# Optimization experiments

Measured on AMD Instinct MI355X. Metric: run time of the kernel, lower is better.

## Reference

```python
import jax, jax.numpy as jnp
import numpy as np

DIM = 32
B, H, W = 4, 256, 256


def conv1x1(x, w, b):
    # x: [B,C,H,W], w: [O,C], b: [O]
    return jnp.einsum('bchw,oc->bohw', x, w) + b[None, :, None, None]


def conv3x3(x, w, b):
    # x: [B,C,H,W], w: [O,C,3,3]
    out = jax.lax.conv_general_dilated(
        x, w, window_strides=(1, 1), padding='SAME',
        dimension_numbers=('NCHW', 'OIHW', 'NCHW'))
    return out + b[None, :, None, None]


def fft2d(x):
    # fft2 over last two dims, then fftshift over ALL dims (torch default)
    f = jnp.fft.fftshift(jnp.fft.fft2(x, norm='ortho'))
    return jnp.concatenate([f.real, f.imag], axis=1)  # [B,2C,H,W]


def ifft2d(x):
    f = jnp.fft.ifftshift(x)  # over ALL dims (torch default)
    re, im = jnp.split(f, 2, axis=1)
    c = jax.lax.complex(re, im)
    return jnp.abs(jnp.fft.ifft2(c, norm='ortho'))  # [B,C,H,W]


def setup_inputs() -> dict:
    key = jax.random.key(0)
    ks = jax.random.split(key, 16)
    C = DIM
    s = 0.02  # small init keeps the global-HW dot products in a sane softmax range
    inp = {
        'x': jax.random.normal(ks[0], (B, C, H, W), jnp.float32),
        'y': jax.random.normal(ks[1], (B, C, H, W), jnp.float32),
        'wq': jax.random.normal(ks[2], (C, C), jnp.float32) * s,
        'bq': jnp.zeros((C,), jnp.float32),
        'wk': jax.random.normal(ks[3], (C, C), jnp.float32) * s,
        'bk': jnp.zeros((C,), jnp.float32),
        'wv': jax.random.normal(ks[4], (C, C), jnp.float32) * s,
        'bv': jnp.zeros((C,), jnp.float32),
        'wd': jax.random.normal(ks[5], (C, C), jnp.float32) * s,
        'bd': jnp.zeros((C,), jnp.float32),
        'wc': jax.random.normal(ks[6], (2 * C, 2 * C, 3, 3), jnp.float32) * s,
        'bc': jnp.zeros((2 * C,), jnp.float32),
        'wi': jax.random.normal(ks[7], (2 * C, 2 * C, 3, 3), jnp.float32) * s,
        'bi': jnp.zeros((2 * C,), jnp.float32),
    }
    return inp


def reference(x, y, wq, bq, wk, bk, wv, bv, wd, bd, wc, bc, wi, bi):
    b, c, h, w = x.shape
    xq = conv1x1(x, wq, bq).reshape(b, c, h * w)            # [B,C,HW]
    dft = conv3x3(fft2d(conv1x1(y, wd, bd)), wc, bc)        # [B,2C,H,W]
    yk, yv = jnp.split(dft, 2, axis=1)
    yk = conv1x1(yk, wk, bk).reshape(b, c, h * w)
    yv = conv1x1(yv, wv, bv).reshape(b, c, h * w)
    att = jnp.einsum('bcn,bdn->bcd', xq, yk)                # [B,C,C]
    att = jax.nn.softmax(att, axis=1)                       # softmax over dim=1 (as in torch)
    out = jnp.einsum('bcd,bdn->bcn', att, yv).reshape(b, c, h, w)
    out = out + ifft2d(conv3x3(jax.nn.relu(dft), wi, bi))
    return out
```

## Files before the change

kernel.cpp:

```cpp
#include <hip/hip_runtime.h>
#include <math.h>

#define HW_ (256*256)
#define CH 32
#define CH2 64
#define BATCH 4

typedef short bf16x8 __attribute__((ext_vector_type(8)));
typedef float f32x4 __attribute__((ext_vector_type(4)));

__device__ __forceinline__ unsigned short f2bf(float f) {
    union { float f; unsigned u; } v; v.f = f;
    unsigned r = v.u + 0x7fffu + ((v.u >> 16) & 1u);
    return (unsigned short)(r >> 16);
}
__device__ __forceinline__ float bf2f(unsigned h) {
    union { unsigned u; float f; } v; v.u = h << 16;
    return v.f;
}

__device__ __forceinline__ int ctof_slot(int s) {
    return s < 16 ? s + 16 : s < 32 ? s + 32 : s < 48 ? s - 32 : s - 16;
}

__device__ __forceinline__ float2 cmul(float2 a, float2 b) {
    return make_float2(a.x*b.x - a.y*b.y, a.x*b.y + a.y*b.x);
}

__device__ __forceinline__ uint4 relu_bf16x8(uint4 v) {
    unsigned* pv = (unsigned*)&v;
    #pragma unroll
    for (int q = 0; q < 4; ++q) {
        unsigned a = pv[q];
        unsigned lo = a & 0xffffu, hi = a >> 16;
        if (lo & 0x8000u) lo = 0;
        if (hi & 0x8000u) hi = 0;
        pv[q] = lo | (hi << 16);
    }
    return v;
}

__device__ __forceinline__ void build_tw4(float2* tw, float sign) {
    int tid = threadIdx.x;
    float ang = sign * 6.2831853071795864769f * (float)tid / 256.0f;
    float s, c; sincosf(ang, &s, &c);
    tw[tid] = make_float2(c, s);
}

template<int SGN>
__device__ __forceinline__ void fft16_reg(float2* x, const float2* tw) {
    float2 u[16];
    #pragma unroll
    for (int m0 = 0; m0 < 4; ++m0) {
        float2 x0 = x[m0], x1 = x[m0+4], x2 = x[m0+8], x3 = x[m0+12];
        float2 t0 = make_float2(x0.x+x2.x, x0.y+x2.y);
        float2 t1 = make_float2(x0.x-x2.x, x0.y-x2.y);
        float2 t2 = make_float2(x1.x+x3.x, x1.y+x3.y);
        float2 t3 = make_float2(x1.x-x3.x, x1.y-x3.y);
        float2 r  = make_float2(-SGN*t3.y, SGN*t3.x);
        u[m0*4+0] = make_float2(t0.x+t2.x, t0.y+t2.y);
        u[m0*4+1] = make_float2(t1.x+r.x,  t1.y+r.y);
        u[m0*4+2] = make_float2(t0.x-t2.x, t0.y-t2.y);
        u[m0*4+3] = make_float2(t1.x-r.x,  t1.y-r.y);
    }
    #pragma unroll
    for (int m0 = 1; m0 < 4; ++m0)
        #pragma unroll
        for (int a = 1; a < 4; ++a)
            u[m0*4+a] = cmul(u[m0*4+a], tw[(16*m0*a) & 255]);
    #pragma unroll
    for (int a = 0; a < 4; ++a) {
        float2 x0 = u[a], x1 = u[4+a], x2 = u[8+a], x3 = u[12+a];
        float2 t0 = make_float2(x0.x+x2.x, x0.y+x2.y);
        float2 t1 = make_float2(x0.x-x2.x, x0.y-x2.y);
        float2 t2 = make_float2(x1.x+x3.x, x1.y+x3.y);
        float2 t3 = make_float2(x1.x-x3.x, x1.y-x3.y);
        float2 r  = make_float2(-SGN*t3.y, SGN*t3.x);
        x[a]    = make_float2(t0.x+t2.x, t0.y+t2.y);
        x[a+4]  = make_float2(t1.x+r.x,  t1.y+r.y);
        x[a+8]  = make_float2(t0.x-t2.x, t0.y-t2.y);
        x[a+12] = make_float2(t1.x-r.x,  t1.y-r.y);
    }
}

template<int SGN>
__device__ __forceinline__ void fft_core16(float2* A, const float2* tw) {
    const int tid = threadIdx.x;
    const int l = tid >> 4;
    const int d = tid & 15;
    const int base = l*257;
    float2 x[16];
    #pragma unroll
    for (int n1 = 0; n1 < 16; ++n1) x[n1] = A[base + n1*16 + d];
    fft16_reg<SGN>(x, tw);
    #pragma unroll
    for (int k0 = 1; k0 < 16; ++k0) x[k0] = cmul(x[k0], tw[d*k0]);
    #pragma unroll
    for (int k0 = 0; k0 < 16; ++k0) A[base + k0*16 + ((d + k0) & 15)] = x[k0];
    __syncthreads();
    #pragma unroll
    for (int n0 = 0; n0 < 16; ++n0) x[n0] = A[base + d*16 + ((n0 + d) & 15)];
    fft16_reg<SGN>(x, tw);
    #pragma unroll
    for (int k1 = 0; k1 < 16; ++k1) A[base + d + k1*16] = x[k1];
    __syncthreads();
}

__global__ __launch_bounds__(256) void k_fft_fwd1(const unsigned short* __restrict__ yd, ushort2* __restrict__ CAt) {
    __shared__ float2 A[16*257];
    __shared__ float2 tw[256];
    build_tw4(tw, -1.0f);
    int blk = blockIdx.x;
    int bc = blk >> 4, h0 = (blk & 15) << 4;
    const float sc = 1.0f/16.0f;
    const unsigned short* src = yd + (size_t)bc*HW_ + (size_t)h0*256;
    for (int idx = threadIdx.x; idx < 16*64; idx += 256) {
        int l = idx >> 6, w4 = (idx & 63) << 2;
        uint2 v = *(const uint2*)(src + l*256 + w4);
        A[l*257 + w4+0] = make_float2(bf2f(v.x & 0xffffu)*sc, 0.0f);
        A[l*257 + w4+1] = make_float2(bf2f(v.x >> 16)*sc, 0.0f);
        A[l*257 + w4+2] = make_float2(bf2f(v.y & 0xffffu)*sc, 0.0f);
        A[l*257 + w4+3] = make_float2(bf2f(v.y >> 16)*sc, 0.0f);
    }
    __syncthreads();
    fft_core16<-1>(A, tw);
    int t = threadIdx.x;
    unsigned short pk[32];
    #pragma unroll
    for (int l = 0; l < 16; ++l) {
        float2 v = A[l*257 + t];
        pk[2*l]   = f2bf(v.x);
        pk[2*l+1] = f2bf(v.y);
    }
    uint4* d4 = (uint4*)(CAt + (size_t)bc*HW_ + (size_t)t*256 + h0);
    const uint4* s4 = (const uint4*)pk;
    d4[0] = s4[0]; d4[1] = s4[1]; d4[2] = s4[2]; d4[3] = s4[3];
}

__global__ __launch_bounds__(256) void k_fft_fwd2(const ushort2* __restrict__ CAt, unsigned short* __restrict__ FSH) {
    __shared__ float2 A[16*257];
    __shared__ float2 tw[256];
    build_tw4(tw, -1.0f);
    int blk = blockIdx.x;
    int b = blk >> 9, chalf = (blk >> 8) & 1, w = blk & 255;
    const float sc = 1.0f/16.0f;
    const ushort2* src = CAt + (((size_t)(b*32 + chalf*16))*256 + w)*256;
    for (int idx = threadIdx.x; idx < 16*256; idx += 256) {
        int l = idx >> 8, h = idx & 255;
        ushort2 v = src[(size_t)l*HW_ + h];
        A[l*257 + h] = make_float2(bf2f(v.x)*sc, bf2f(v.y)*sc);
    }
    __syncthreads();
    fft_core16<-1>(A, tw);
    int t = threadIdx.x;
    int bt = (b + 2) & 3;
    int ht = (t + 128) & 255;
    int wt = (w + 128) & 255;
    unsigned short pk[32];
    #pragma unroll
    for (int l = 0; l < 16; ++l) {
        float2 v = A[l*257 + t];
        pk[l]      = f2bf(v.x);
        pk[16 + l] = f2bf(v.y);
    }
    unsigned short* dst = FSH + ((((size_t)bt*256 + ht)*256 + wt)*64 + chalf*32);
    uint4* d4 = (uint4*)dst;
    const uint4* s4 = (const uint4*)pk;
    d4[0] = s4[0]; d4[1] = s4[1]; d4[2] = s4[2]; d4[3] = s4[3];
}

__global__ __launch_bounds__(256) void k_wpack2(const float* __restrict__ wc, const float* __restrict__ wi,
                                                unsigned short* __restrict__ d1, unsigned short* __restrict__ d2) {
    int i = blockIdx.x*256 + threadIdx.x;
    int half = i >= 36864;
    int j = i - half*36864;
    int tap = j >> 12, rem = j & 4095, oc = rem >> 6, s = rem & 63;
    if (half) {
        d2[j] = f2bf(wi[((size_t)(oc*64 + s))*9 + tap]);
    } else {
        int ic = ctof_slot(s);
        d1[j] = f2bf(wc[((size_t)(oc*64 + ic))*9 + tap]);
    }
}

template<int MODE>
__global__ __launch_bounds__(256) void k_conv3(const unsigned short* __restrict__ in_cl,
                                               const unsigned short* __restrict__ wpk,
                                               const float* __restrict__ bias,
                                               unsigned short* __restrict__ outp) {
    __shared__ __align__(16) char Xs[2112*16];
    __shared__ __align__(16) char Ws[1536*16];
    int tid = threadIdx.x;
    int blk = blockIdx.x;
    int wseg = blk & 3, hg = (blk >> 2) & 63, b = blk >> 8;
    int h0 = hg*4, w0 = wseg*64;

    const uint4* wsrc = (const uint4*)wpk;

    for (int gl = tid; gl < 2112; gl += 256) {
        int slot = gl / 528;
        int rem  = gl - slot*528;
        int col  = rem >> 3, hseg = rem & 7;
        int hh = h0 - 1 + slot;
        int wcol = w0 - 1 + col;
        uint4 v = make_uint4(0,0,0,0);
        if (hh >= 0 && hh < 256 && wcol >= 0 && wcol < 256) {
            v = *(const uint4*)(in_cl + (((size_t)(b*256 + hh)*256 + wcol)*64) + hseg*8);
            if (MODE == 1) v = relu_bf16x8(v);
        }
        *(uint4*)(Xs + ((gl << 4) ^ ((col & 7) << 4))) = v;
    }
    #pragma unroll
    for (int q = 0; q < 6; ++q) {
        int gw = tid + q*256;
        int oc = (gw >> 3) & 63;
        *(uint4*)(Ws + ((gw << 4) ^ ((oc & 7) << 4))) = wsrc[gw];
    }
    __syncthreads();

    int lane = tid & 63;
    int wv = tid >> 6;
    int l16 = lane & 15, lq = lane >> 4;

    f32x4 acc[4][4];
    #pragma unroll
    for (int i = 0; i < 4; ++i)
        #pragma unroll
        for (int j = 0; j < 4; ++j) acc[i][j] = (f32x4)0.0f;

    for (int dy = 0; dy < 3; ++dy) {
        uint4 xr0 = make_uint4(0,0,0,0), xr1 = make_uint4(0,0,0,0), xr2 = make_uint4(0,0,0,0);
        uint4 wr[6];
        if (dy < 2) {
            int hh = h0 + dy + 2;
            bool hv = hh < 256;
            {
                int gl = tid;
                int col = gl >> 3, hseg = gl & 7;
                int wcol = w0 - 1 + col;
                if (hv && wcol >= 0 && wcol < 256)
                    xr0 = *(const uint4*)(in_cl + (((size_t)(b*256 + hh)*256 + wcol)*64) + hseg*8);
            }
            {
                int gl = tid + 256;
                int col = gl >> 3, hseg = gl & 7;
                int wcol = w0 - 1 + col;
                if (hv && wcol >= 0 && wcol < 256)
                    xr1 = *(const uint4*)(in_cl + (((size_t)(b*256 + hh)*256 + wcol)*64) + hseg*8);
            }
            if (tid < 16) {
                int gl = tid + 512;
                int col = gl >> 3, hseg = gl & 7;
                int wcol = w0 - 1 + col;
                if (hv && wcol < 256)
                    xr2 = *(const uint4*)(in_cl + (((size_t)(b*256 + hh)*256 + wcol)*64) + hseg*8);
            }
            #pragma unroll
            for (int q = 0; q < 6; ++q)
                wr[q] = wsrc[(dy+1)*1536 + tid + q*256];
        }

        int slot = (wv + dy) & 3;
        #pragma unroll
        for (int dx = 0; dx < 3; ++dx) {
            #pragma unroll
            for (int kk = 0; kk < 2; ++kk) {
                int hseg = kk*4 + lq;
                bf16x8 xf[4], wf[4];
                #pragma unroll
                for (int j = 0; j < 4; ++j) {
                    int col = j*16 + l16 + dx;
                    int g = slot*528 + col*8 + hseg;
                    xf[j] = *(const bf16x8*)(Xs + ((g << 4) ^ ((col & 7) << 4)));
                }
                #pragma unroll
                for (int i = 0; i < 4; ++i) {
                    int oc = i*16 + l16;
                    int lw = dx*512 + oc*8 + hseg;
                    wf[i] = *(const bf16x8*)(Ws + ((lw << 4) ^ ((oc & 7) << 4)));
                    #pragma unroll
                    for (int j = 0; j < 4; ++j) {
                        if (MODE == 0)
                            acc[i][j] = __builtin_amdgcn_mfma_f32_16x16x32_bf16(wf[i], xf[j], acc[i][j], 0, 0, 0);
                        else
                            acc[i][j] = __builtin_amdgcn_mfma_f32_16x16x32_bf16(xf[j], wf[i], acc[i][j], 0, 0, 0);
                    }
                }
            }
        }

        if (dy < 2) {
            __syncthreads();
            int slotn = (dy + 3) & 3;
            {
                int gl = tid;
                int col = gl >> 3;
                uint4 v = (MODE == 1) ? relu_bf16x8(xr0) : xr0;
                int g = slotn*528 + gl;
                *(uint4*)(Xs + ((g << 4) ^ ((col & 7) << 4))) = v;
            }
            {
                int gl = tid + 256;
                int col = gl >> 3;
                uint4 v = (MODE == 1) ? relu_bf16x8(xr1) : xr1;
                int g = slotn*528 + gl;
                *(uint4*)(Xs + ((g << 4) ^ ((col & 7) << 4))) = v;
            }
            if (tid < 16) {
                int gl = tid + 512;
                int col = gl >> 3;
                uint4 v = (MODE == 1) ? relu_bf16x8(xr2) : xr2;
                int g = slotn*528 + gl;
                *(uint4*)(Xs + ((g << 4) ^ ((col & 7) << 4))) = v;
            }
            #pragma unroll
            for (int q = 0; q < 6; ++q) {
                int gw = tid + q*256;
                int oc = (gw >> 3) & 63;
                *(uint4*)(Ws + ((gw << 4) ^ ((oc & 7) << 4))) = wr[q];
            }
            __syncthreads();
        }
    }

    int h = h0 + wv;
    if (MODE == 0) {
        #pragma unroll
        for (int j = 0; j < 4; ++j) {
            int px = w0 + j*16 + l16;
            unsigned short* orow = outp + (((size_t)b*256 + h)*256 + px)*64;
            #pragma unroll
            for (int i = 0; i < 4; ++i) {
                int oc0 = i*16 + lq*4;
                float4 bv = *(const float4*)(bias + oc0);
                unsigned short c0 = f2bf(acc[i][j][0] + bv.x);
                unsigned short c1 = f2bf(acc[i][j][1] + bv.y);
                unsigned short c2 = f2bf(acc[i][j][2] + bv.z);
                unsigned short c3 = f2bf(acc[i][j][3] + bv.w);
                uint2 u;
                u.x = (unsigned)c0 | ((unsigned)c1 << 16);
                u.y = (unsigned)c2 | ((unsigned)c3 << 16);
                *(uint2*)(orow + oc0) = u;
            }
        }
    } else {
        #pragma unroll
        for (int i = 0; i < 4; ++i) {
            int oc = i*16 + l16;
            float bv = bias[oc];
            unsigned short* oplane = outp + ((size_t)b*64 + oc)*HW_ + (size_t)h*256;
            #pragma unroll
            for (int j = 0; j < 4; ++j) {
                int px0 = w0 + j*16 + lq*4;
                unsigned short c0 = f2bf(acc[i][j][0] + bv);
                unsigned short c1 = f2bf(acc[i][j][1] + bv);
                unsigned short c2 = f2bf(acc[i][j][2] + bv);
                unsigned short c3 = f2bf(acc[i][j][3] + bv);
                uint2 u;
                u.x = (unsigned)c0 | ((unsigned)c1 << 16);
                u.y = (unsigned)c2 | ((unsigned)c3 << 16);
                *(uint2*)(oplane + px0) = u;
            }
        }
    }
}

__global__ __launch_bounds__(256) void k_conv1x1(const float* __restrict__ in, const float* __restrict__ w,
                                                 const float* __restrict__ bias, unsigned short* __restrict__ out) {
    __shared__ float ts[32*257];
    int blk = blockIdx.x; int b = blk >> 8, h = blk & 255;
    int tid = threadIdx.x;
    const float* src = in + (size_t)b*CH*HW_ + (size_t)h*256;
    for (int idx = tid; idx < 32*256; idx += 256) {
        int c = idx >> 8, ww = idx & 255;
        ts[c*257 + ww] = src[(size_t)c*HW_ + ww];
    }
    __syncthreads();
    float acc[32];
    #pragma unroll
    for (int o = 0; o < 32; ++o) acc[o] = bias[o];
    for (int c = 0; c < 32; ++c) {
        float v = ts[c*257 + tid];
        #pragma unroll
        for (int o = 0; o < 32; ++o) acc[o] += w[o*32 + c] * v;
    }
    unsigned short* dst = out + (size_t)b*CH*HW_ + (size_t)h*256 + tid;
    #pragma unroll
    for (int o = 0; o < 32; ++o) dst[(size_t)o*HW_] = f2bf(acc[o]);
}

__global__ __launch_bounds__(256) void k_gram(const float* __restrict__ x, const unsigned short* __restrict__ dcl,
                                              float* __restrict__ Mpart, float* __restrict__ Sxp, float* __restrict__ Sdp) {
    __shared__ float mred[1024];
    __shared__ float sxred[32];
    __shared__ float sdred[32];
    int blk = blockIdx.x;
    int b = blk >> 7, chunk = blk & 127;
    int tid = threadIdx.x, lane = tid & 63, wv = tid >> 6;
    int l16 = lane & 15, lq = lane >> 4;
    for (int idx = tid; idx < 1024; idx += 256) mred[idx] = 0.0f;
    if (tid < 32) { sxred[tid] = 0.0f; sdred[tid] = 0.0f; }
    __syncthreads();

    const float* xb0 = x + (size_t)b*CH*HW_ + (size_t)l16*HW_;
    const float* xb1 = xb0 + (size_t)16*HW_;
    const unsigned short* db = dcl + (size_t)b*HW_*64;

    f32x4 acc[2][2];
    #pragma unroll
    for (int i = 0; i < 2; ++i)
        #pragma unroll
        for (int j = 0; j < 2; ++j) acc[i][j] = (f32x4)0.0f;
    float sx0 = 0, sx1 = 0, sd0 = 0, sd1 = 0;

    int pxw = chunk*512 + wv*128;
    #pragma unroll
    for (int ks = 0; ks < 4; ++ks) {
        int px = pxw + ks*32 + lq*8;
        float4 xa = *(const float4*)(xb0 + px);
        float4 xc = *(const float4*)(xb0 + px + 4);
        float4 ya = *(const float4*)(xb1 + px);
        float4 yc = *(const float4*)(xb1 + px + 4);
        bf16x8 a0, a1, b0, b1;
        const float* pxa = (const float*)&xa;
        const float* pxc = (const float*)&xc;
        const float* pya = (const float*)&ya;
        const float* pyc = (const float*)&yc;
        #pragma unroll
        for (int j = 0; j < 4; ++j) {
            a0[j]   = (short)f2bf(pxa[j]);  sx0 += pxa[j];
            a0[4+j] = (short)f2bf(pxc[j]);  sx0 += pxc[j];
            a1[j]   = (short)f2bf(pya[j]);  sx1 += pya[j];
            a1[4+j] = (short)f2bf(pyc[j]);  sx1 += pyc[j];
        }
        const unsigned short* dbp = db + (size_t)px*64 + l16;
        #pragma unroll
        for (int j = 0; j < 8; ++j) {
            unsigned short v0 = dbp[j*64];
            unsigned short v1 = dbp[j*64 + 16];
            b0[j] = (short)v0;  sd0 += bf2f(v0);
            b1[j] = (short)v1;  sd1 += bf2f(v1);
        }
        acc[0][0] = __builtin_amdgcn_mfma_f32_16x16x32_bf16(a0, b0, acc[0][0], 0, 0, 0);
        acc[0][1] = __builtin_amdgcn_mfma_f32_16x16x32_bf16(a0, b1, acc[0][1], 0, 0, 0);
        acc[1][0] = __builtin_amdgcn_mfma_f32_16x16x32_bf16(a1, b0, acc[1][0], 0, 0, 0);
        acc[1][1] = __builtin_amdgcn_mfma_f32_16x16x32_bf16(a1, b1, acc[1][1], 0, 0, 0);
    }

    #pragma unroll
    for (int fi = 0; fi < 2; ++fi)
        #pragma unroll
        for (int fj = 0; fj < 2; ++fj)
            #pragma unroll
            for (int r = 0; r < 4; ++r)
                atomicAdd(&mred[(fi*16 + lq*4 + r)*32 + fj*16 + l16], acc[fi][fj][r]);

    sx0 += __shfl_xor(sx0, 16); sx0 += __shfl_xor(sx0, 32);
    sx1 += __shfl_xor(sx1, 16); sx1 += __shfl_xor(sx1, 32);
    sd0 += __shfl_xor(sd0, 16); sd0 += __shfl_xor(sd0, 32);
    sd1 += __shfl_xor(sd1, 16); sd1 += __shfl_xor(sd1, 32);
    if (lane < 16) {
        atomicAdd(&sxred[l16], sx0);
        atomicAdd(&sxred[l16 + 16], sx1);
        atomicAdd(&sdred[l16], sd0);
        atomicAdd(&sdred[l16 + 16], sd1);
    }
    __syncthreads();

    float* mp = Mpart + ((size_t)(b*128 + chunk))*1024;
    for (int idx = tid; idx < 1024; idx += 256) mp[idx] = mred[idx];
    if (tid < 32) {
        Sxp[(b*128 + chunk)*32 + tid] = sxred[tid];
        Sdp[(b*128 + chunk)*32 + tid] = sdred[tid];
    }
}

__global__ __launch_bounds__(256) void k_att(const float* __restrict__ Mpart, const float* __restrict__ Sxp,
                                              const float* __restrict__ Sdp,
                                              const float* __restrict__ wq, const float* __restrict__ bq,
                                              const float* __restrict__ wk, const float* __restrict__ bk,
                                              const float* __restrict__ wv, const float* __restrict__ bv,
                                              float* __restrict__ att2, float* __restrict__ sout) {
    __shared__ float Mls[1024], T1[1024], attls[32*33];
    __shared__ float wqs[1024], wks[1024], wvs[1024];
    __shared__ float q1[32], k1[32], sxs[32], sds[32];
    int tid = threadIdx.x;
    int b = blockIdx.x;
    for (int idx = tid; idx < 1024; idx += 256) { wqs[idx] = wq[idx]; wks[idx] = wk[idx]; wvs[idx] = wv[idx]; }
    #pragma unroll
    for (int q = 0; q < 4; ++q) {
        int o = tid + q*256;
        float s = 0;
        for (int c = 0; c < 128; ++c) s += Mpart[((size_t)(b*128 + c))*1024 + o];
        Mls[o] = s;
    }
    if (tid < 32) { float s = 0; for (int c = 0; c < 128; ++c) s += Sxp[(b*128 + c)*32 + tid]; sxs[tid] = s; }
    else if (tid < 64) { int e = tid - 32; float s = 0; for (int c = 0; c < 128; ++c) s += Sdp[(b*128 + c)*32 + e]; sds[e] = s; }
    __syncthreads();
    if (tid < 32) { float s=0; for (int a=0;a<32;++a) s += wqs[tid*32+a]*sxs[a]; q1[tid]=s; }
    else if (tid < 64) { int d=tid-32; float s=0; for (int e=0;e<32;++e) s += wks[d*32+e]*sds[e]; k1[d]=s; }
    for (int idx = tid; idx < 1024; idx += 256) {
        int c = idx >> 5, e = idx & 31;
        float s = 0;
        for (int a=0;a<32;++a) s += wqs[c*32+a]*Mls[a*32+e];
        T1[idx] = s;
    }
    __syncthreads();
    for (int idx = tid; idx < 1024; idx += 256) {
        int c = idx >> 5, d = idx & 31;
        float s = 0;
        for (int e=0;e<32;++e) s += T1[c*32+e]*wks[d*32+e];
        s += bq[c]*k1[d] + bk[d]*q1[c] + 65536.0f*bq[c]*bk[d];
        attls[c*33+d] = s;
    }
    __syncthreads();
    if (tid < 32) {
        int d = tid;
        float mx = -1e30f;
        for (int c=0;c<32;++c) mx = fmaxf(mx, attls[c*33+d]);
        float sum = 0;
        for (int c=0;c<32;++c) { float e_ = expf(attls[c*33+d]-mx); attls[c*33+d]=e_; sum+=e_; }
        float inv = 1.0f/sum;
        for (int c=0;c<32;++c) attls[c*33+d] *= inv;
    }
    __syncthreads();
    for (int idx = tid; idx < 1024; idx += 256) {
        int c = idx >> 5, e = idx & 31;
        float s = 0;
        for (int d=0; d<32; ++d) s += attls[c*33+d]*wvs[d*32+e];
        att2[b*1024 + idx] = s;
    }
    if (tid < 32) {
        float s=0; for (int d=0;d<32;++d) s += attls[tid*33+d]*bv[d];
        sout[b*32+tid] = s;
    }
}

__global__ __launch_bounds__(256) void k_fft_inv1(const unsigned short* __restrict__ G, ushort2* __restrict__ Z1T) {
    __shared__ float2 A[16*257];
    __shared__ float2 tw[256];
    build_tw4(tw, 1.0f);
    int blk = blockIdx.x;
    int bc = blk >> 4, w0 = (blk & 15) << 4;
    int b = bc >> 5, c = bc & 31;
    int bs = (b + 2) & 3;
    const float sc = 1.0f/16.0f;
    const unsigned short* gre = G + ((size_t)(bs*CH2 + c + 32))*HW_;
    const unsigned short* gim = G + ((size_t)(bs*CH2 + c))*HW_;
    for (int idx = threadIdx.x; idx < 16*256; idx += 256) {
        int h = idx >> 4, l = idx & 15;
        int hs = (h + 128) & 255;
        int ws = (w0 + l + 128) & 255;
        A[l*257 + h] = make_float2(bf2f(gre[(size_t)hs*256 + ws])*sc, bf2f(gim[(size_t)hs*256 + ws])*sc);
    }
    __syncthreads();
    fft_core16<1>(A, tw);
    ushort2* dst = Z1T + (size_t)bc*HW_;
    for (int idx = threadIdx.x; idx < 16*256; idx += 256) {
        int l = idx >> 8, h = idx & 255;
        float2 v = A[l*257 + h];
        dst[(size_t)(w0 + l)*256 + h] = make_ushort2(f2bf(v.x), f2bf(v.y));
    }
}

__global__ __launch_bounds__(256) void k_fft_inv2(const ushort2* __restrict__ Z1T, unsigned short* __restrict__ Mag) {
    __shared__ float2 A[16*257];
    __shared__ float2 tw[256];
    build_tw4(tw, 1.0f);
    int blk = blockIdx.x;
    int bc = blk >> 4, h0 = (blk & 15) << 4;
    const float sc = 1.0f/16.0f;
    const ushort2* src = Z1T + (size_t)bc*HW_ + h0;
    for (int idx = threadIdx.x; idx < 16*256; idx += 256) {
        int w = idx >> 4, l = idx & 15;
        ushort2 v = src[(size_t)w*256 + l];
        A[l*257 + w] = make_float2(bf2f(v.x)*sc, bf2f(v.y)*sc);
    }
    __syncthreads();
    fft_core16<1>(A, tw);
    unsigned short* dst = Mag + (size_t)bc*HW_ + (size_t)h0*256;
    for (int idx = threadIdx.x; idx < 16*256; idx += 256) {
        int l = idx >> 8, w = idx & 255;
        float2 v = A[l*257 + w];
        dst[l*256 + w] = f2bf(sqrtf(v.x*v.x + v.y*v.y));
    }
}

__global__ __launch_bounds__(256) void k_out(const unsigned short* __restrict__ dcl, const float* __restrict__ att2,
                                             const float* __restrict__ sv, const unsigned short* __restrict__ Mag,
                                             float* __restrict__ out) {
    __shared__ __align__(16) float A2ls[1024];
    __shared__ float svls[32];
    int blk = blockIdx.x; int b = blk >> 8, h = blk & 255;
    int tid = threadIdx.x;
    for (int idx = tid; idx < 1024; idx += 256) A2ls[idx] = att2[b*1024 + idx];
    if (tid < 32) svls[tid] = sv[b*32 + tid];
    __syncthreads();
    int px = tid;
    const uint4* dvp = (const uint4*)(dcl + ((((size_t)b*256 + h)*256 + px)*64 + 32));
    uint4 d0 = dvp[0], d1 = dvp[1];
    unsigned u[8] = {d0.x, d0.y, d0.z, d0.w, d1.x, d1.y, d1.z, d1.w};
    float dv[32];
    #pragma unroll
    for (int i = 0; i < 8; ++i) {
        dv[2*i]   = bf2f(u[i] & 0xffffu);
        dv[2*i+1] = bf2f(u[i] >> 16);
    }
    float accv[32];
    #pragma unroll
    for (int c = 0; c < 32; ++c) accv[c] = svls[c];
    #pragma unroll
    for (int q = 0; q < 8; ++q) {
        #pragma unroll
        for (int c = 0; c < 32; ++c) {
            float4 a4 = *(const float4*)&A2ls[c*32 + q*4];
            accv[c] += a4.x*dv[q*4] + a4.y*dv[q*4+1] + a4.z*dv[q*4+2] + a4.w*dv[q*4+3];
        }
    }
    const unsigned short* mb = Mag + (size_t)b*CH*HW_ + (size_t)h*256 + px;
    float* ob = out + (size_t)b*CH*HW_ + (size_t)h*256 + px;
    #pragma unroll
    for (int c = 0; c < 32; ++c) ob[(size_t)c*HW_] = accv[c] + bf2f(mb[(size_t)c*HW_]);
}

extern "C" void kernel_launch(void* const* d_in, const int* in_sizes, int n_in,
                              void* d_out, int out_size, void* d_ws, size_t ws_size,
                              hipStream_t stream) {
    const float* x  = (const float*)d_in[0];
    const float* y  = (const float*)d_in[1];
    const float* wq = (const float*)d_in[2];
    const float* bq = (const float*)d_in[3];
    const float* wk = (const float*)d_in[4];
    const float* bk = (const float*)d_in[5];
    const float* wv = (const float*)d_in[6];
    const float* bv = (const float*)d_in[7];
    const float* wd = (const float*)d_in[8];
    const float* bd = (const float*)d_in[9];
    const float* wc = (const float*)d_in[10];
    const float* bc = (const float*)d_in[11];
    const float* wi = (const float*)d_in[12];
    const float* bi = (const float*)d_in[13];
    float* out = (float*)d_out;

    char* ws = (char*)d_ws;
    size_t o = 0;
    unsigned short* R1   = (unsigned short*)(ws + o); o += (size_t)BATCH*CH*HW_*2;
    ushort2*        CAt  = (ushort2*)(ws + o);        o += (size_t)BATCH*CH*HW_*4;
    unsigned short* FSHc = (unsigned short*)(ws + o); o += (size_t)BATCH*CH2*HW_*2;
    unsigned short* DFTc = (unsigned short*)(ws + o); o += (size_t)BATCH*CH2*HW_*2;
    unsigned short* Gpl  = (unsigned short*)(ws + o); o += (size_t)BATCH*CH2*HW_*2;
    unsigned short* wpk1 = (unsigned short*)(ws + o); o += 9*64*64*2;
    unsigned short* wpk2 = (unsigned short*)(ws + o); o += 9*64*64*2;
    float*          Mpart= (float*)(ws + o);          o += (size_t)512*1024*4;
    float*          Sxp  = (float*)(ws + o);          o += 512*32*4;
    float*          Sdp  = (float*)(ws + o);          o += 512*32*4;
    float*          A2b  = (float*)(ws + o);          o += 4096*4;
    float*          Svb  = (float*)(ws + o);          o += 128*4;
    if (ws_size < o) return;

    ushort2*        Z1T = CAt;
    unsigned short* Mag = R1;

    k_wpack2<<<288, 256, 0, stream>>>(wc, wi, wpk1, wpk2);
    k_conv1x1<<<1024, 256, 0, stream>>>(y, wd, bd, R1);
    k_fft_fwd1<<<2048, 256, 0, stream>>>(R1, CAt);
    k_fft_fwd2<<<2048, 256, 0, stream>>>(CAt, FSHc);
    k_conv3<0><<<1024, 256, 0, stream>>>(FSHc, wpk1, bc, DFTc);
    k_conv3<1><<<1024, 256, 0, stream>>>(DFTc, wpk2, bi, Gpl);
    k_gram<<<512, 256, 0, stream>>>(x, DFTc, Mpart, Sxp, Sdp);
    k_att<<<4, 256, 0, stream>>>(Mpart, Sxp, Sdp, wq, bq, wk, bk, wv, bv, A2b, Svb);
    k_fft_inv1<<<2048, 256, 0, stream>>>(Gpl, Z1T);
    k_fft_inv2<<<2048, 256, 0, stream>>>(Z1T, Mag);
    k_out<<<1024, 256, 0, stream>>>(DFTc, A2b, Svb, Mag, out);
}
```

Measured before the change: 278.3 us.

## Stage conv3 epilogue and gram inputs through LDS, fuse weight pack into conv1x1

The conv3 epilogue now writes its tile into swizzled shared memory, then issues coalesced 16-byte global stores for both the channel-last and planar output layouts. k_gram stages x and DFT tiles in shared memory per 128-pixel step, so the strided 2-byte gathers from the channel-last buffer become vector loads plus an LDS transpose. The weight-pack kernel is merged into the conv1x1 launch as extra blocks, removing one launch. The cost is extra LDS traffic and more barriers in both kernels.

```diff
diff --git a/kernel.cpp b/kernel.cpp
--- a/kernel.cpp
+++ b/kernel.cpp
@@ -169,18 +169,44 @@
     d4[0] = s4[0]; d4[1] = s4[1]; d4[2] = s4[2]; d4[3] = s4[3];
 }
 
-__global__ __launch_bounds__(256) void k_wpack2(const float* __restrict__ wc, const float* __restrict__ wi,
-                                                unsigned short* __restrict__ d1, unsigned short* __restrict__ d2) {
-    int i = blockIdx.x*256 + threadIdx.x;
-    int half = i >= 36864;
-    int j = i - half*36864;
-    int tap = j >> 12, rem = j & 4095, oc = rem >> 6, s = rem & 63;
-    if (half) {
-        d2[j] = f2bf(wi[((size_t)(oc*64 + s))*9 + tap]);
-    } else {
-        int ic = ctof_slot(s);
-        d1[j] = f2bf(wc[((size_t)(oc*64 + ic))*9 + tap]);
-    }
+__global__ __launch_bounds__(256) void k_conv1x1w(const float* __restrict__ in, const float* __restrict__ w,
+                                                  const float* __restrict__ bias, unsigned short* __restrict__ out,
+                                                  const float* __restrict__ wc, const float* __restrict__ wi,
+                                                  unsigned short* __restrict__ d1, unsigned short* __restrict__ d2) {
+    __shared__ float ts[32*257];
+    int blk = blockIdx.x;
+    int tid = threadIdx.x;
+    if (blk >= 1024) {
+        int i = (blk - 1024)*256 + tid;
+        int half = i >= 36864;
+        int j = i - half*36864;
+        int tap = j >> 12, rem = j & 4095, oc = rem >> 6, s = rem & 63;
+        if (half) {
+            d2[j] = f2bf(wi[((size_t)(oc*64 + s))*9 + tap]);
+        } else {
+            int ic = ctof_slot(s);
+            d1[j] = f2bf(wc[((size_t)(oc*64 + ic))*9 + tap]);
+        }
+        return;
+    }
+    int b = blk >> 8, h = blk & 255;
+    const float* src = in + (size_t)b*CH*HW_ + (size_t)h*256;
+    for (int idx = tid; idx < 32*256; idx += 256) {
+        int c = idx >> 8, ww = idx & 255;
+        ts[c*257 + ww] = src[(size_t)c*HW_ + ww];
+    }
+    __syncthreads();
+    float acc[32];
+    #pragma unroll
+    for (int o = 0; o < 32; ++o) acc[o] = bias[o];
+    for (int c = 0; c < 32; ++c) {
+        float v = ts[c*257 + tid];
+        #pragma unroll
+        for (int o = 0; o < 32; ++o) acc[o] += w[o*32 + c] * v;
+    }
+    unsigned short* dst = out + (size_t)b*CH*HW_ + (size_t)h*256 + tid;
+    #pragma unroll
+    for (int o = 0; o < 32; ++o) dst[(size_t)o*HW_] = f2bf(acc[o]);
 }
 
 template<int MODE>
@@ -323,12 +349,13 @@
         }
     }
 
-    int h = h0 + wv;
+    __syncthreads();
+    char* Es = Xs;
     if (MODE == 0) {
         #pragma unroll
         for (int j = 0; j < 4; ++j) {
-            int px = w0 + j*16 + l16;
-            unsigned short* orow = outp + (((size_t)b*256 + h)*256 + px)*64;
+            int px = j*16 + l16;
+            int rowswz = (px & 7) << 4;
             #pragma unroll
             for (int i = 0; i < 4; ++i) {
                 int oc0 = i*16 + lq*4;
@@ -340,18 +367,19 @@
                 uint2 u;
                 u.x = (unsigned)c0 | ((unsigned)c1 << 16);
                 u.y = (unsigned)c2 | ((unsigned)c3 << 16);
-                *(uint2*)(orow + oc0) = u;
+                int byte = wv*8192 + px*128 + oc0*2;
+                *(uint2*)(Es + (byte ^ rowswz)) = u;
             }
         }
     } else {
         #pragma unroll
         for (int i = 0; i < 4; ++i) {
             int oc = i*16 + l16;
+            int rowswz = (oc & 7) << 4;
             float bv = bias[oc];
-            unsigned short* oplane = outp + ((size_t)b*64 + oc)*HW_ + (size_t)h*256;
             #pragma unroll
             for (int j = 0; j < 4; ++j) {
-                int px0 = w0 + j*16 + lq*4;
+                int px0 = j*16 + lq*4;
                 unsigned short c0 = f2bf(acc[i][j][0] + bv);
                 unsigned short c1 = f2bf(acc[i][j][1] + bv);
                 unsigned short c2 = f2bf(acc[i][j][2] + bv);
@@ -359,38 +387,31 @@
                 uint2 u;
                 u.x = (unsigned)c0 | ((unsigned)c1 << 16);
                 u.y = (unsigned)c2 | ((unsigned)c3 << 16);
-                *(uint2*)(oplane + px0) = u;
-            }
-        }
-    }
-}
-
-__global__ __launch_bounds__(256) void k_conv1x1(const float* __restrict__ in, const float* __restrict__ w,
-                                                 const float* __restrict__ bias, unsigned short* __restrict__ out) {
-    __shared__ float ts[32*257];
-    int blk = blockIdx.x; int b = blk >> 8, h = blk & 255;
-    int tid = threadIdx.x;
-    const float* src = in + (size_t)b*CH*HW_ + (size_t)h*256;
-    for (int idx = tid; idx < 32*256; idx += 256) {
-        int c = idx >> 8, ww = idx & 255;
-        ts[c*257 + ww] = src[(size_t)c*HW_ + ww];
-    }
-    __syncthreads();
-    float acc[32];
-    #pragma unroll
-    for (int o = 0; o < 32; ++o) acc[o] = bias[o];
-    for (int c = 0; c < 32; ++c) {
-        float v = ts[c*257 + tid];
-        #pragma unroll
-        for (int o = 0; o < 32; ++o) acc[o] += w[o*32 + c] * v;
-    }
-    unsigned short* dst = out + (size_t)b*CH*HW_ + (size_t)h*256 + tid;
-    #pragma unroll
-    for (int o = 0; o < 32; ++o) dst[(size_t)o*HW_] = f2bf(acc[o]);
+                int byte = wv*8192 + oc*128 + px0*2;
+                *(uint2*)(Es + (byte ^ rowswz)) = u;
+            }
+        }
+    }
+    __syncthreads();
+    #pragma unroll
+    for (int q = 0; q < 8; ++q) {
+        int off = (q*256 + tid)*16;
+        uint4 v = *(const uint4*)(Es + (off ^ (((off >> 7) & 7) << 4)));
+        int wvp = off >> 13;
+        int row = (off >> 7) & 63;
+        int bir = off & 127;
+        if (MODE == 0) {
+            *(uint4*)(outp + (((size_t)(b*256 + h0 + wvp)*256 + w0 + row)*64) + (bir >> 1)) = v;
+        } else {
+            *(uint4*)(outp + ((size_t)(b*64 + row)*HW_) + (size_t)(h0 + wvp)*256 + w0 + (bir >> 1)) = v;
+        }
+    }
 }
 
 __global__ __launch_bounds__(256) void k_gram(const float* __restrict__ x, const unsigned short* __restrict__ dcl,
                                               float* __restrict__ Mpart, float* __restrict__ Sxp, float* __restrict__ Sdp) {
+    __shared__ __align__(16) float xs[32*132];
+    __shared__ __align__(16) unsigned short dst_[32*136];
     __shared__ float mred[1024];
     __shared__ float sxred[32];
     __shared__ float sdred[32];
@@ -400,10 +421,8 @@
     int l16 = lane & 15, lq = lane >> 4;
     for (int idx = tid; idx < 1024; idx += 256) mred[idx] = 0.0f;
     if (tid < 32) { sxred[tid] = 0.0f; sdred[tid] = 0.0f; }
-    __syncthreads();
-
-    const float* xb0 = x + (size_t)b*CH*HW_ + (size_t)l16*HW_;
-    const float* xb1 = xb0 + (size_t)16*HW_;
+
+    const float* xb = x + (size_t)b*CH*HW_;
     const unsigned short* db = dcl + (size_t)b*HW_*64;
 
     f32x4 acc[2][2];
@@ -413,39 +432,58 @@
         for (int j = 0; j < 2; ++j) acc[i][j] = (f32x4)0.0f;
     float sx0 = 0, sx1 = 0, sd0 = 0, sd1 = 0;
 
-    int pxw = chunk*512 + wv*128;
-    #pragma unroll
-    for (int ks = 0; ks < 4; ++ks) {
-        int px = pxw + ks*32 + lq*8;
-        float4 xa = *(const float4*)(xb0 + px);
-        float4 xc = *(const float4*)(xb0 + px + 4);
-        float4 ya = *(const float4*)(xb1 + px);
-        float4 yc = *(const float4*)(xb1 + px + 4);
-        bf16x8 a0, a1, b0, b1;
-        const float* pxa = (const float*)&xa;
-        const float* pxc = (const float*)&xc;
-        const float* pya = (const float*)&ya;
-        const float* pyc = (const float*)&yc;
-        #pragma unroll
-        for (int j = 0; j < 4; ++j) {
-            a0[j]   = (short)f2bf(pxa[j]);  sx0 += pxa[j];
-            a0[4+j] = (short)f2bf(pxc[j]);  sx0 += pxc[j];
-            a1[j]   = (short)f2bf(pya[j]);  sx1 += pya[j];
-            a1[4+j] = (short)f2bf(pyc[j]);  sx1 += pyc[j];
-        }
-        const unsigned short* dbp = db + (size_t)px*64 + l16;
-        #pragma unroll
-        for (int j = 0; j < 8; ++j) {
-            unsigned short v0 = dbp[j*64];
-            unsigned short v1 = dbp[j*64 + 16];
-            b0[j] = (short)v0;  sd0 += bf2f(v0);
-            b1[j] = (short)v1;  sd1 += bf2f(v1);
-        }
-        acc[0][0] = __builtin_amdgcn_mfma_f32_16x16x32_bf16(a0, b0, acc[0][0], 0, 0, 0);
-        acc[0][1] = __builtin_amdgcn_mfma_f32_16x16x32_bf16(a0, b1, acc[0][1], 0, 0, 0);
-        acc[1][0] = __builtin_amdgcn_mfma_f32_16x16x32_bf16(a1, b0, acc[1][0], 0, 0, 0);
-        acc[1][1] = __builtin_amdgcn_mfma_f32_16x16x32_bf16(a1, b1, acc[1][1], 0, 0, 0);
-    }
+    for (int q4 = 0; q4 < 4; ++q4) {
+        int px0 = chunk*512 + q4*128;
+        __syncthreads();
+        #pragma unroll
+        for (int p = 0; p < 4; ++p) {
+            int g = tid + p*256;
+            int c = g >> 5, k4 = (g & 31) << 2;
+            *(float4*)&xs[c*132 + k4] = *(const float4*)(xb + (size_t)c*HW_ + px0 + k4);
+        }
+        #pragma unroll
+        for (int p = 0; p < 2; ++p) {
+            int g = tid + p*256;
+            int px = g >> 2, quad = g & 3;
+            uint4 v = *(const uint4*)(db + (size_t)(px0 + px)*64 + quad*8);
+            const unsigned short* pv = (const unsigned short*)&v;
+            #pragma unroll
+            for (int u = 0; u < 8; ++u) dst_[(quad*8 + u)*136 + px] = pv[u];
+        }
+        __syncthreads();
+        #pragma unroll
+        for (int ks = 0; ks < 4; ++ks) {
+            int k0 = ks*32 + lq*8;
+            float4 xa = *(const float4*)&xs[l16*132 + k0];
+            float4 xc = *(const float4*)&xs[l16*132 + k0 + 4];
+            float4 ya = *(const float4*)&xs[(16+l16)*132 + k0];
+            float4 yc = *(const float4*)&xs[(16+l16)*132 + k0 + 4];
+            bf16x8 a0, a1;
+            const float* pxa = (const float*)&xa;
+            const float* pxc = (const float*)&xc;
+            const float* pya = (const float*)&ya;
+            const float* pyc = (const float*)&yc;
+            #pragma unroll
+            for (int j = 0; j < 4; ++j) {
+                a0[j]   = (short)f2bf(pxa[j]);  sx0 += pxa[j];
+                a0[4+j] = (short)f2bf(pxc[j]);  sx0 += pxc[j];
+                a1[j]   = (short)f2bf(pya[j]);  sx1 += pya[j];
+                a1[4+j] = (short)f2bf(pyc[j]);  sx1 += pyc[j];
+            }
+            bf16x8 b0 = *(const bf16x8*)&dst_[l16*136 + k0];
+            bf16x8 b1 = *(const bf16x8*)&dst_[(16+l16)*136 + k0];
+            #pragma unroll
+            for (int j = 0; j < 8; ++j) {
+                sd0 += bf2f((unsigned short)b0[j]);
+                sd1 += bf2f((unsigned short)b1[j]);
+            }
+            acc[0][0] = __builtin_amdgcn_mfma_f32_16x16x32_bf16(a0, b0, acc[0][0], 0, 0, 0);
+            acc[0][1] = __builtin_amdgcn_mfma_f32_16x16x32_bf16(a0, b1, acc[0][1], 0, 0, 0);
+            acc[1][0] = __builtin_amdgcn_mfma_f32_16x16x32_bf16(a1, b0, acc[1][0], 0, 0, 0);
+            acc[1][1] = __builtin_amdgcn_mfma_f32_16x16x32_bf16(a1, b1, acc[1][1], 0, 0, 0);
+        }
+    }
+    __syncthreads();
 
     #pragma unroll
     for (int fi = 0; fi < 2; ++fi)
@@ -661,8 +699,7 @@
     ushort2*        Z1T = CAt;
     unsigned short* Mag = R1;
 
-    k_wpack2<<<288, 256, 0, stream>>>(wc, wi, wpk1, wpk2);
-    k_conv1x1<<<1024, 256, 0, stream>>>(y, wd, bd, R1);
+    k_conv1x1w<<<1312, 256, 0, stream>>>(y, wd, bd, R1, wc, wi, wpk1, wpk2);
     k_fft_fwd1<<<2048, 256, 0, stream>>>(R1, CAt);
     k_fft_fwd2<<<2048, 256, 0, stream>>>(CAt, FSHc);
     k_conv3<0><<<1024, 256, 0, stream>>>(FSHc, wpk1, bc, DFTc);
```

New measurement: 275.5 us. No clear change (-1.0%).
